# Kernel optimization log

Hardware: AMD Instinct MI355X
Metric: run time of the kernel (lower is better)

The kernel has to match this reference:

```python
import jax, jax.numpy as jnp
import numpy as np

N_HEAD = 16

def setup_inputs() -> dict:
    key = jax.random.key(0)
    k1, k2, k3 = jax.random.split(key, 3)
    B, T, C = 4, 2048, 1024
    x = jax.random.normal(k1, (B, T, C), dtype=jnp.float32)
    W_qkv = jax.random.normal(k2, (3 * C, C), dtype=jnp.float32) * 0.02
    W_o = jax.random.normal(k3, (C, C), dtype=jnp.float32) * (0.02 / np.sqrt(2.0))
    return {"x": x, "W_qkv": W_qkv, "W_o": W_o}

def reference(x, W_qkv, W_o):
    B, T, C = x.shape
    H = N_HEAD
    d_k = C // H
    # combined qkv projection (torch Linear: y = x @ W^T)
    qkv = x @ W_qkv.T                      # (B, T, 3C)
    q, k, v = jnp.split(qkv, 3, axis=-1)
    def split_heads(t):
        return t.reshape(B, T, H, d_k).transpose(0, 2, 1, 3)  # (B, H, T, d_k)
    q, k, v = split_heads(q), split_heads(k), split_heads(v)
    scale = 1.0 / jnp.sqrt(jnp.asarray(d_k, dtype=x.dtype))
    scores = jnp.einsum('bhqd,bhkd->bhqk', q, k) * scale      # (B, H, T, T)
    causal = jnp.tril(jnp.ones((T, T), dtype=bool))           # True = keep
    scores = jnp.where(causal[None, None], scores, -jnp.inf)
    attn = jax.nn.softmax(scores, axis=-1)                    # no NaNs under causal mask
    out = jnp.einsum('bhqk,bhkd->bhqd', attn, v)              # (B, H, T, d_k)
    out = out.transpose(0, 2, 1, 3).reshape(B, T, C)
    return out @ W_o.T
```

## Files before the change

kernel.cpp:

```cpp
#include <hip/hip_runtime.h>
#include <hip/hip_bf16.h>
#include <cstdint>

typedef __bf16 bf16;
typedef __bf16 bf16x8 __attribute__((ext_vector_type(8)));
typedef float f32x4 __attribute__((ext_vector_type(4)));

#define MFMA16(A, B, C) __builtin_amdgcn_mfma_f32_16x16x32_bf16((A), (B), (C), 0, 0, 0)

__device__ __forceinline__ void async16(const bf16* g, bf16* l) {
    __builtin_amdgcn_global_load_lds(
        (const __attribute__((address_space(1))) void*)g,
        (__attribute__((address_space(3))) void*)l, 16, 0, 0);
}

__global__ void cvt_all(const float* __restrict__ x, const float* __restrict__ wq,
                        const float* __restrict__ wo, bf16* __restrict__ xb,
                        bf16* __restrict__ wqb, bf16* __restrict__ wob) {
    const int bid = blockIdx.x;
    const float* s;
    bf16* d;
    int off;
    if (bid < 4096)      { s = x;  d = xb;  off = bid; }
    else if (bid < 5632) { s = wq; d = wqb; off = bid - 4096; }
    else                 { s = wo; d = wob; off = bid - 5632; }
    const size_t i = ((size_t)off * 256 + threadIdx.x) * 8;
    const float4 a = *(const float4*)(s + i);
    const float4 b2 = *(const float4*)(s + i + 4);
    bf16x8 r;
    r[0] = (bf16)a.x; r[1] = (bf16)a.y; r[2] = (bf16)a.z; r[3] = (bf16)a.w;
    r[4] = (bf16)b2.x; r[5] = (bf16)b2.y; r[6] = (bf16)b2.z; r[7] = (bf16)b2.w;
    *(bf16x8*)(d + i) = r;
}

template <int MODE>
__launch_bounds__(256, 3)
__global__ void gemm_nt(const bf16* __restrict__ A, const bf16* __restrict__ Bm,
                        void* __restrict__ O0, bf16* __restrict__ O1,
                        bf16* __restrict__ O2, int N, int K) {
    __shared__ alignas(16) bf16 As[128 * 64];
    __shared__ alignas(16) bf16 Bs[128 * 64];

    const int t = threadIdx.x;
    const int w = t >> 6, l = t & 63, quad = l >> 4, l15 = l & 15;
    const int wm = w & 1, wn = w >> 1;
    const int m0 = blockIdx.y * 128, n0 = blockIdx.x * 128;

    f32x4 acc[4][4] = {};

    const int srow = t >> 3, sch = t & 7;
    const bf16* ga = A + (size_t)(m0 + srow) * K + sch * 8;
    const bf16* gb = Bm + (size_t)(n0 + srow) * K + sch * 8;

    for (int kt = 0; kt < K; kt += 64) {
        __syncthreads();
#pragma unroll
        for (int i = 0; i < 4; i++) {
            async16(ga + (size_t)i * 32 * K + kt, &As[(i * 256 + t) * 8]);
            async16(gb + (size_t)i * 32 * K + kt, &Bs[(i * 256 + t) * 8]);
        }
        __syncthreads();

#pragma unroll
        for (int s = 0; s < 2; s++) {
            bf16x8 af[4], bfr[4];
#pragma unroll
            for (int im = 0; im < 4; im++)
                af[im] = *(const bf16x8*)&As[(wm * 64 + im * 16 + l15) * 64 + s * 32 + quad * 8];
#pragma unroll
            for (int in = 0; in < 4; in++)
                bfr[in] = *(const bf16x8*)&Bs[(wn * 64 + in * 16 + l15) * 64 + s * 32 + quad * 8];
#pragma unroll
            for (int im = 0; im < 4; im++)
#pragma unroll
                for (int in = 0; in < 4; in++)
                    acc[im][in] = MFMA16(af[im], bfr[in], acc[im][in]);
        }
    }

    if (MODE == 0) {
        bf16* Q0 = (bf16*)O0;
#pragma unroll
        for (int in = 0; in < 4; in++) {
            const int n = n0 + wn * 64 + in * 16;
            const int sel = n >> 10;
            const int c = n & 1023;
            const int h = c >> 6;
            const int dd = c & 63;
            bf16* dst = (sel == 0) ? Q0 : ((sel == 1) ? O1 : O2);
#pragma unroll
            for (int im = 0; im < 4; im++) {
#pragma unroll
                for (int r = 0; r < 4; r++) {
                    const int m = m0 + wm * 64 + im * 16 + quad * 4 + r;
                    const int b = m >> 11, tt = m & 2047;
                    dst[((size_t)(b * 16 + h) * 2048 + tt) * 64 + dd + l15] =
                        (bf16)acc[im][in][r];
                }
            }
        }
    } else {
        float* Of = (float*)O0;
#pragma unroll
        for (int im = 0; im < 4; im++) {
#pragma unroll
            for (int in = 0; in < 4; in++) {
#pragma unroll
                for (int r = 0; r < 4; r++) {
                    const int m = m0 + wm * 64 + im * 16 + quad * 4 + r;
                    const int n = n0 + wn * 64 + in * 16 + l15;
                    Of[(size_t)m * N + n] = acc[im][in][r];
                }
            }
        }
    }
}

__launch_bounds__(256, 4)
__global__ void vtrans(const bf16* __restrict__ V, bf16* __restrict__ Vt) {
    __shared__ alignas(16) bf16 Ls[64 * 72];
    const int t = threadIdx.x, bh = blockIdx.y, tt = blockIdx.x;
#pragma unroll
    for (int i = 0; i < 2; i++) {
        const int id = i * 256 + t, r = id >> 3, c = id & 7;
        *(bf16x8*)&Ls[r * 72 + c * 8] =
            *(const bf16x8*)&V[((size_t)bh * 2048 + tt * 64 + r) * 64 + c * 8];
    }
    __syncthreads();
#pragma unroll
    for (int i = 0; i < 2; i++) {
        const int id = i * 256 + t, d = id >> 3, c = id & 7;
        bf16x8 v;
#pragma unroll
        for (int j = 0; j < 8; j++) v[j] = Ls[(c * 8 + j) * 72 + d];
        *(bf16x8*)&Vt[((size_t)bh * 64 + d) * 2048 + tt * 64 + c * 8] = v;
    }
}

__launch_bounds__(256, 4)
__global__ void attn_fwd(const bf16* __restrict__ Q, const bf16* __restrict__ Kk,
                         const bf16* __restrict__ Vt, bf16* __restrict__ O) {
    __shared__ alignas(16) bf16 Ks[64 * 72];
    __shared__ alignas(16) bf16 Vs[64 * 72];

    const int t = threadIdx.x, w = t >> 6, l = t & 63;
    const int quad = l >> 4, l15 = l & 15;
    const int bh = blockIdx.y, pair = blockIdx.x;
    const int b = bh >> 4, h = bh & 15;
    const int sr = t >> 3, sc = t & 7;

    const bf16* Qbase = Q + (size_t)bh * 2048 * 64;
    const bf16* Kbase = Kk + (size_t)bh * 2048 * 64;
    const bf16* Vbase = Vt + (size_t)bh * 64 * 2048;

    const int qt0 = pair, qt1 = 31 - pair;

    int kr[4];
#pragma unroll
    for (int nt = 0; nt < 4; nt++)
        kr[nt] = (nt >> 1) * 32 + (l15 >> 2) * 8 + (nt & 1) * 4 + (l15 & 3);

    bf16x8 aq[2][2];
#pragma unroll
    for (int hf = 0; hf < 2; hf++) {
        const int qrow = (hf ? qt1 : qt0) * 64 + w * 16 + l15;
        aq[hf][0] = *(const bf16x8*)&Qbase[(size_t)qrow * 64 + quad * 8];
        aq[hf][1] = *(const bf16x8*)&Qbase[(size_t)qrow * 64 + 32 + quad * 8];
#pragma unroll
        for (int j = 0; j < 8; j++) {
            aq[hf][0][j] = aq[hf][0][j] * (bf16)0.1803369f;
            aq[hf][1][j] = aq[hf][1][j] * (bf16)0.1803369f;
        }
    }

    bf16x8 ones;
#pragma unroll
    for (int j = 0; j < 8; j++) ones[j] = (bf16)1.0f;

    f32x4 liacc[2] = {};
    f32x4 oa[2][4] = {};

    for (int kt = 0; kt <= qt1; kt++) {
        bf16x8 rk0 = *(const bf16x8*)&Kbase[(size_t)(kt * 64 + sr) * 64 + sc * 8];
        bf16x8 rk1 = *(const bf16x8*)&Kbase[(size_t)(kt * 64 + sr + 32) * 64 + sc * 8];
        bf16x8 rv0 = *(const bf16x8*)&Vbase[(size_t)sr * 2048 + kt * 64 + sc * 8];
        bf16x8 rv1 = *(const bf16x8*)&Vbase[(size_t)(sr + 32) * 2048 + kt * 64 + sc * 8];
        __syncthreads();
        *(bf16x8*)&Ks[sr * 72 + sc * 8] = rk0;
        *(bf16x8*)&Ks[(sr + 32) * 72 + sc * 8] = rk1;
        *(bf16x8*)&Vs[sr * 72 + sc * 8] = rv0;
        *(bf16x8*)&Vs[(sr + 32) * 72 + sc * 8] = rv1;
        __syncthreads();

        const bool do0 = (kt <= qt0);

        bf16x8 ap[2][2];
#pragma unroll
        for (int np = 0; np < 2; np++) {
            bf16x8 ka[2][2];
#pragma unroll
            for (int i = 0; i < 2; i++) {
                ka[i][0] = *(const bf16x8*)&Ks[kr[2 * np + i] * 72 + quad * 8];
                ka[i][1] = *(const bf16x8*)&Ks[kr[2 * np + i] * 72 + 32 + quad * 8];
            }
#pragma unroll
            for (int hf = 0; hf < 2; hf++) {
                if (hf == 0 && !do0) continue;
                const bool diag = (kt == (hf ? qt1 : qt0));
#pragma unroll
                for (int i = 0; i < 2; i++) {
                    f32x4 s = {};
                    s = MFMA16(ka[i][0], aq[hf][0], s);
                    s = MFMA16(ka[i][1], aq[hf][1], s);
                    const int kbase = np * 32 + quad * 8 + i * 4;
#pragma unroll
                    for (int r = 0; r < 4; r++) {
                        float x = s[r];
                        if (diag && (kbase + r) > (w * 16 + l15)) x = -1e30f;
                        ap[hf][np][i * 4 + r] = (bf16)__builtin_amdgcn_exp2f(x);
                    }
                }
            }
        }

#pragma unroll
        for (int s2 = 0; s2 < 2; s2++) {
            if (do0) liacc[0] = MFMA16(ap[0][s2], ones, liacc[0]);
            liacc[1] = MFMA16(ap[1][s2], ones, liacc[1]);
#pragma unroll
            for (int dt = 0; dt < 4; dt++) {
                bf16x8 bv = *(const bf16x8*)&Vs[(dt * 16 + l15) * 72 + s2 * 32 + quad * 8];
                if (do0) oa[0][dt] = MFMA16(ap[0][s2], bv, oa[0][dt]);
                oa[1][dt] = MFMA16(ap[1][s2], bv, oa[1][dt]);
            }
        }
    }

#pragma unroll
    for (int hf = 0; hf < 2; hf++) {
        const int qt = hf ? qt1 : qt0;
#pragma unroll
        for (int r = 0; r < 4; r++) {
            const float inv = __builtin_amdgcn_rcpf(liacc[hf][r]);
            const int m = b * 2048 + qt * 64 + w * 16 + quad * 4 + r;
#pragma unroll
            for (int dt = 0; dt < 4; dt++) {
                O[(size_t)m * 1024 + h * 64 + dt * 16 + l15] = (bf16)(oa[hf][dt][r] * inv);
            }
        }
    }
}

extern "C" void kernel_launch(void* const* d_in, const int* in_sizes, int n_in,
                              void* d_out, int out_size, void* d_ws, size_t ws_size,
                              hipStream_t stream) {
    const float* x = (const float*)d_in[0];
    const float* wqkv = (const float*)d_in[1];
    const float* wo = (const float*)d_in[2];

    const size_t SZ = (size_t)8192 * 1024;
    bf16* xb = (bf16*)d_ws;
    bf16* wqb = xb + SZ;
    bf16* wob = wqb + (size_t)3072 * 1024;
    bf16* Qw = wob + (size_t)1024 * 1024;
    bf16* Kw = Qw + SZ;
    bf16* Vw = Kw + SZ;
    bf16* Vtw = xb;

    dim3 blk(256);
    cvt_all<<<6144, blk, 0, stream>>>(x, wqkv, wo, xb, wqb, wob);
    gemm_nt<0><<<dim3(24, 64), blk, 0, stream>>>(xb, wqb, Qw, Kw, Vw, 3072, 1024);
    vtrans<<<dim3(32, 64), blk, 0, stream>>>(Vw, Vtw);
    attn_fwd<<<dim3(16, 64), blk, 0, stream>>>(Qw, Kw, Vtw, Vw);
    gemm_nt<1><<<dim3(8, 64), blk, 0, stream>>>(Vw, wob, d_out, nullptr, nullptr, 1024, 1024);
}
```

Before: 250.1 us.

## Replace GEMM with double-buffered 128x256 swizzled 512-thread kernel

Rewrites the projection GEMM to use 128x256 tiles with 512 threads and double-buffered LDS. Loads for the next K tile are issued asynchronously, split across two barrier phases so they overlap the MFMAs. LDS chunks are XOR-swizzled to cut bank conflicts, and a block-index remap spreads tiles across XCDs. It also raises wave priority around the MFMA bursts. In exchange it uses more LDS and has fewer blocks per CU, and correctness depends on hand-placed waitcnt counts.

```diff
diff --git a/kernel.cpp b/kernel.cpp
--- a/kernel.cpp
+++ b/kernel.cpp
@@ -34,48 +34,125 @@
 }
 
 template <int MODE>
-__launch_bounds__(256, 3)
-__global__ void gemm_nt(const bf16* __restrict__ A, const bf16* __restrict__ Bm,
+__launch_bounds__(512, 2)
+__global__ void gemm256(const bf16* __restrict__ A, const bf16* __restrict__ Bm,
                         void* __restrict__ O0, bf16* __restrict__ O1,
                         bf16* __restrict__ O2, int N, int K) {
-    __shared__ alignas(16) bf16 As[128 * 64];
-    __shared__ alignas(16) bf16 Bs[128 * 64];
-
-    const int t = threadIdx.x;
-    const int w = t >> 6, l = t & 63, quad = l >> 4, l15 = l & 15;
-    const int wm = w & 1, wn = w >> 1;
-    const int m0 = blockIdx.y * 128, n0 = blockIdx.x * 128;
+    __shared__ alignas(16) bf16 As[2][128 * 64];
+    __shared__ alignas(16) bf16 Bs[2][2][128 * 64];
+
+    const int t = threadIdx.x, w = t >> 6, l = t & 63;
+    const int quad = l >> 4, l15 = l & 15;
+    const int wm = w >> 2, wn = w & 3;
+
+    const int nwg = gridDim.x;
+    const int wg = ((int)blockIdx.x & 7) * (nwg >> 3) + ((int)blockIdx.x >> 3);
+    const int NBN = N >> 8;
+    const int m0 = (wg / NBN) * 128, n0 = (wg % NBN) * 256;
+
+    const int NT = K >> 6;
+
+    int a_src[2], a_dst[2];
+#pragma unroll
+    for (int j = 0; j < 2; j++) {
+        const int id = j * 512 + t;
+        const int row = id >> 3, c = id & 7;
+        a_src[j] = (m0 + row) * K + ((c ^ (row & 7)) << 3);
+        a_dst[j] = id << 3;
+    }
+    int b_src[2], b_h[2], b_dst[2];
+#pragma unroll
+    for (int j = 0; j < 2; j++) {
+        const int id = j * 512 + t;
+        const int u = id >> 8, rr = (id >> 3) & 31, c = id & 7;
+        b_src[j] = (n0 + u * 64 + rr) * K + ((c ^ (rr & 7)) << 3);
+        b_h[j] = u >> 1;
+        b_dst[j] = ((u & 1) << 12) + ((id & 255) << 3);
+    }
+
+    const int sw = l15 & 7;
+    int aoff[4][2], boff[4][2];
+#pragma unroll
+    for (int im = 0; im < 4; im++) {
+        const int r = wm * 64 + im * 16 + l15;
+#pragma unroll
+        for (int s2 = 0; s2 < 2; s2++)
+            aoff[im][s2] = r * 64 + (((s2 * 4 + quad) ^ sw) << 3);
+    }
+    const int bhalf = wn >> 1;
+#pragma unroll
+    for (int in = 0; in < 4; in++) {
+        const int r = (wn & 1) * 64 + (in >> 1) * 32 + (in & 1) * 16 + l15;
+#pragma unroll
+        for (int s2 = 0; s2 < 2; s2++)
+            boff[in][s2] = r * 64 + (((s2 * 4 + quad) ^ sw) << 3);
+    }
 
     f32x4 acc[4][4] = {};
 
-    const int srow = t >> 3, sch = t & 7;
-    const bf16* ga = A + (size_t)(m0 + srow) * K + sch * 8;
-    const bf16* gb = Bm + (size_t)(n0 + srow) * K + sch * 8;
-
-    for (int kt = 0; kt < K; kt += 64) {
-        __syncthreads();
-#pragma unroll
-        for (int i = 0; i < 4; i++) {
-            async16(ga + (size_t)i * 32 * K + kt, &As[(i * 256 + t) * 8]);
-            async16(gb + (size_t)i * 32 * K + kt, &Bs[(i * 256 + t) * 8]);
-        }
-        __syncthreads();
-
-#pragma unroll
-        for (int s = 0; s < 2; s++) {
-            bf16x8 af[4], bfr[4];
-#pragma unroll
-            for (int im = 0; im < 4; im++)
-                af[im] = *(const bf16x8*)&As[(wm * 64 + im * 16 + l15) * 64 + s * 32 + quad * 8];
-#pragma unroll
-            for (int in = 0; in < 4; in++)
-                bfr[in] = *(const bf16x8*)&Bs[(wn * 64 + in * 16 + l15) * 64 + s * 32 + quad * 8];
-#pragma unroll
-            for (int im = 0; im < 4; im++)
-#pragma unroll
-                for (int in = 0; in < 4; in++)
-                    acc[im][in] = MFMA16(af[im], bfr[in], acc[im][in]);
-        }
+    async16(A + a_src[0], &As[0][a_dst[0]]);
+    async16(A + a_src[1], &As[0][a_dst[1]]);
+    async16(Bm + b_src[0], &Bs[0][b_h[0]][b_dst[0]]);
+    async16(Bm + b_src[1], &Bs[0][b_h[1]][b_dst[1]]);
+    async16(Bm + b_src[0] + 32 * K, &Bs[0][b_h[0]][b_dst[0] + 2048]);
+    async16(Bm + b_src[1] + 32 * K, &Bs[0][b_h[1]][b_dst[1] + 2048]);
+
+    for (int tile = 0; tile < NT; ++tile) {
+        const int cb = tile & 1, pb = cb ^ 1;
+        const bool nl = (tile + 1 < NT);
+        const int ks = (tile + 1) << 6;
+
+        asm volatile("s_waitcnt vmcnt(2)" ::: "memory");
+        __builtin_amdgcn_s_barrier();
+        if (nl) {
+            async16(A + a_src[0] + ks, &As[pb][a_dst[0]]);
+            async16(A + a_src[1] + ks, &As[pb][a_dst[1]]);
+            async16(Bm + b_src[0] + ks, &Bs[pb][b_h[0]][b_dst[0]]);
+        }
+        bf16x8 af[4][2], bf0[2][2];
+#pragma unroll
+        for (int im = 0; im < 4; im++)
+#pragma unroll
+            for (int s2 = 0; s2 < 2; s2++)
+                af[im][s2] = *(const bf16x8*)&As[cb][aoff[im][s2]];
+#pragma unroll
+        for (int i2 = 0; i2 < 2; i2++)
+#pragma unroll
+            for (int s2 = 0; s2 < 2; s2++)
+                bf0[i2][s2] = *(const bf16x8*)&Bs[cb][bhalf][boff[i2][s2]];
+        __builtin_amdgcn_s_setprio(1);
+#pragma unroll
+        for (int im = 0; im < 4; im++)
+#pragma unroll
+            for (int i2 = 0; i2 < 2; i2++) {
+                acc[im][i2] = MFMA16(af[im][0], bf0[i2][0], acc[im][i2]);
+                acc[im][i2] = MFMA16(af[im][1], bf0[i2][1], acc[im][i2]);
+            }
+        __builtin_amdgcn_s_setprio(0);
+
+        if (nl) asm volatile("s_waitcnt vmcnt(3)" ::: "memory");
+        else    asm volatile("s_waitcnt vmcnt(0)" ::: "memory");
+        __builtin_amdgcn_s_barrier();
+        if (nl) {
+            async16(Bm + b_src[1] + ks, &Bs[pb][b_h[1]][b_dst[1]]);
+            async16(Bm + b_src[0] + 32 * K + ks, &Bs[pb][b_h[0]][b_dst[0] + 2048]);
+            async16(Bm + b_src[1] + 32 * K + ks, &Bs[pb][b_h[1]][b_dst[1] + 2048]);
+        }
+        bf16x8 bf1[2][2];
+#pragma unroll
+        for (int i2 = 0; i2 < 2; i2++)
+#pragma unroll
+            for (int s2 = 0; s2 < 2; s2++)
+                bf1[i2][s2] = *(const bf16x8*)&Bs[cb][bhalf][boff[2 + i2][s2]];
+        __builtin_amdgcn_s_setprio(1);
+#pragma unroll
+        for (int im = 0; im < 4; im++)
+#pragma unroll
+            for (int i2 = 0; i2 < 2; i2++) {
+                acc[im][2 + i2] = MFMA16(af[im][0], bf1[i2][0], acc[im][2 + i2]);
+                acc[im][2 + i2] = MFMA16(af[im][1], bf1[i2][1], acc[im][2 + i2]);
+            }
+        __builtin_amdgcn_s_setprio(0);
     }
 
     if (MODE == 0) {
@@ -269,8 +346,8 @@
 
     dim3 blk(256);
     cvt_all<<<6144, blk, 0, stream>>>(x, wqkv, wo, xb, wqb, wob);
-    gemm_nt<0><<<dim3(24, 64), blk, 0, stream>>>(xb, wqb, Qw, Kw, Vw, 3072, 1024);
+    gemm256<0><<<dim3(768), dim3(512), 0, stream>>>(xb, wqb, Qw, Kw, Vw, 3072, 1024);
     vtrans<<<dim3(32, 64), blk, 0, stream>>>(Vw, Vtw);
     attn_fwd<<<dim3(16, 64), blk, 0, stream>>>(Qw, Kw, Vtw, Vw);
-    gemm_nt<1><<<dim3(8, 64), blk, 0, stream>>>(Vw, wob, d_out, nullptr, nullptr, 1024, 1024);
-}
+    gemm256<1><<<dim3(256), dim3(512), 0, stream>>>(Vw, wob, d_out, nullptr, nullptr, 1024, 1024);
+}
```

Measured after the change: 274.8 us. 9.9% more time.

## Replace 128x128 GEMM with double-buffered 256x256 tile GEMM using swizzled LDS

Applied to the files above, without the earlier changes.

Rewrites both projection GEMMs to use 256x256 output tiles with 512 threads (8 waves), double-buffered LDS split into k-halves, and global-to-LDS async loads for the next tile interleaved with MFMA on the current one. LDS rows are XOR-swizzled to reduce bank conflicts, and workgroup IDs are remapped across XCDs for L2 locality. The aim is to hide load latency and raise arithmetic intensity in the GEMMs. In exchange it uses 128KB of LDS and more accumulator registers, and the output GEMM launches only 128 workgroups, which may underfill the device.

```diff
diff --git a/kernel.cpp b/kernel.cpp
--- a/kernel.cpp
+++ b/kernel.cpp
@@ -34,86 +34,162 @@
 }
 
 template <int MODE>
-__launch_bounds__(256, 3)
-__global__ void gemm_nt(const bf16* __restrict__ A, const bf16* __restrict__ Bm,
+__launch_bounds__(512, 2)
+__global__ void gemm256(const bf16* __restrict__ A, const bf16* __restrict__ Bm,
                         void* __restrict__ O0, bf16* __restrict__ O1,
                         bf16* __restrict__ O2, int N, int K) {
-    __shared__ alignas(16) bf16 As[128 * 64];
-    __shared__ alignas(16) bf16 Bs[128 * 64];
-
-    const int t = threadIdx.x;
-    const int w = t >> 6, l = t & 63, quad = l >> 4, l15 = l & 15;
-    const int wm = w & 1, wn = w >> 1;
-    const int m0 = blockIdx.y * 128, n0 = blockIdx.x * 128;
-
-    f32x4 acc[4][4] = {};
-
-    const int srow = t >> 3, sch = t & 7;
-    const bf16* ga = A + (size_t)(m0 + srow) * K + sch * 8;
-    const bf16* gb = Bm + (size_t)(n0 + srow) * K + sch * 8;
-
-    for (int kt = 0; kt < K; kt += 64) {
-        __syncthreads();
-#pragma unroll
-        for (int i = 0; i < 4; i++) {
-            async16(ga + (size_t)i * 32 * K + kt, &As[(i * 256 + t) * 8]);
-            async16(gb + (size_t)i * 32 * K + kt, &Bs[(i * 256 + t) * 8]);
-        }
-        __syncthreads();
-
-#pragma unroll
-        for (int s = 0; s < 2; s++) {
-            bf16x8 af[4], bfr[4];
-#pragma unroll
-            for (int im = 0; im < 4; im++)
-                af[im] = *(const bf16x8*)&As[(wm * 64 + im * 16 + l15) * 64 + s * 32 + quad * 8];
-#pragma unroll
-            for (int in = 0; in < 4; in++)
-                bfr[in] = *(const bf16x8*)&Bs[(wn * 64 + in * 16 + l15) * 64 + s * 32 + quad * 8];
-#pragma unroll
-            for (int im = 0; im < 4; im++)
-#pragma unroll
-                for (int in = 0; in < 4; in++)
-                    acc[im][in] = MFMA16(af[im], bfr[in], acc[im][in]);
-        }
+    __shared__ alignas(16) bf16 As[2 * 2 * 8192];
+    __shared__ alignas(16) bf16 Bs[2 * 2 * 8192];
+
+    const int t = threadIdx.x, w = t >> 6, l = t & 63;
+    const int quad = l >> 4, l15 = l & 15;
+    const int wm = w >> 2, wn = w & 3;
+
+    const int nwg = gridDim.x;
+    const int wg = ((int)blockIdx.x & 7) * (nwg >> 3) + ((int)blockIdx.x >> 3);
+    const int NBN = N >> 8;
+    const int m0 = (wg / NBN) * 256, n0 = (wg % NBN) * 256;
+
+    const int NT = K >> 6;
+
+    int a_src[2], b_src[2], sdst[2];
+#pragma unroll
+    for (int jj = 0; jj < 2; jj++) {
+        const int id2 = jj * 512 + t;
+        const int row = id2 >> 2, pc = id2 & 3;
+        const int gcoff = (pc ^ (row & 3)) << 3;
+        a_src[jj] = (m0 + row) * K + gcoff;
+        b_src[jj] = (n0 + row) * K + gcoff;
+        sdst[jj] = id2 << 3;
+    }
+
+    const int pcs = (quad ^ (l15 & 3)) << 3;
+    const int arow = wm * 128 + l15;
+    const int brow = wn * 64 + l15;
+
+    f32x4 acc[8][4] = {};
+
+#define STAGE_A(ktile, buf, kh, jj)                                          \
+    async16(A + a_src[jj] + (ktile) * 64 + (kh) * 32,                        \
+            &As[((((buf) << 1) + (kh)) << 13) + sdst[jj]])
+#define STAGE_B(ktile, buf, kh, jj)                                          \
+    async16(Bm + b_src[jj] + (ktile) * 64 + (kh) * 32,                       \
+            &Bs[((((buf) << 1) + (kh)) << 13) + sdst[jj]])
+
+#define LDA(cb, kh, mf)                                                      \
+    (*(const bf16x8*)&As[((((cb) << 1) + (kh)) << 13) +                      \
+                         ((arow + (mf) * 16) << 5) + pcs])
+#define LDB(cb, kh, nf)                                                      \
+    (*(const bf16x8*)&Bs[((((cb) << 1) + (kh)) << 13) +                      \
+                         ((brow + (nf) * 16) << 5) + pcs])
+
+    STAGE_A(0, 0, 0, 0); STAGE_A(0, 0, 0, 1);
+    STAGE_B(0, 0, 0, 0); STAGE_B(0, 0, 0, 1);
+    STAGE_A(0, 0, 1, 0); STAGE_A(0, 0, 1, 1);
+    STAGE_B(0, 0, 1, 0); STAGE_B(0, 0, 1, 1);
+
+    for (int tile = 0; tile < NT; ++tile) {
+        const int cb = tile & 1, pb = cb ^ 1;
+        const bool nl = (tile + 1 < NT);
+        const int kn = tile + 1;
+        bf16x8 af[4], bfr[4];
+
+        asm volatile("s_waitcnt vmcnt(4)" ::: "memory");
+        __builtin_amdgcn_s_barrier();
+        if (nl) { STAGE_A(kn, pb, 0, 0); STAGE_A(kn, pb, 0, 1); }
+#pragma unroll
+        for (int mf = 0; mf < 4; mf++) af[mf] = LDA(cb, 0, mf);
+#pragma unroll
+        for (int nf = 0; nf < 4; nf++) bfr[nf] = LDB(cb, 0, nf);
+        __builtin_amdgcn_s_setprio(1);
+#pragma unroll
+        for (int mf = 0; mf < 4; mf++)
+#pragma unroll
+            for (int nf = 0; nf < 4; nf++)
+                acc[mf][nf] = MFMA16(af[mf], bfr[nf], acc[mf][nf]);
+        __builtin_amdgcn_s_setprio(0);
+
+        __builtin_amdgcn_s_barrier();
+        if (nl) { STAGE_B(kn, pb, 0, 0); STAGE_B(kn, pb, 0, 1); }
+#pragma unroll
+        for (int mf = 0; mf < 4; mf++) af[mf] = LDA(cb, 0, 4 + mf);
+        __builtin_amdgcn_s_setprio(1);
+#pragma unroll
+        for (int mf = 0; mf < 4; mf++)
+#pragma unroll
+            for (int nf = 0; nf < 4; nf++)
+                acc[4 + mf][nf] = MFMA16(af[mf], bfr[nf], acc[4 + mf][nf]);
+        __builtin_amdgcn_s_setprio(0);
+
+        if (nl) asm volatile("s_waitcnt vmcnt(4)" ::: "memory");
+        else    asm volatile("s_waitcnt vmcnt(0)" ::: "memory");
+        __builtin_amdgcn_s_barrier();
+        if (nl) { STAGE_A(kn, pb, 1, 0); STAGE_A(kn, pb, 1, 1); }
+#pragma unroll
+        for (int mf = 0; mf < 4; mf++) af[mf] = LDA(cb, 1, mf);
+#pragma unroll
+        for (int nf = 0; nf < 4; nf++) bfr[nf] = LDB(cb, 1, nf);
+        __builtin_amdgcn_s_setprio(1);
+#pragma unroll
+        for (int mf = 0; mf < 4; mf++)
+#pragma unroll
+            for (int nf = 0; nf < 4; nf++)
+                acc[mf][nf] = MFMA16(af[mf], bfr[nf], acc[mf][nf]);
+        __builtin_amdgcn_s_setprio(0);
+
+        __builtin_amdgcn_s_barrier();
+        if (nl) { STAGE_B(kn, pb, 1, 0); STAGE_B(kn, pb, 1, 1); }
+#pragma unroll
+        for (int mf = 0; mf < 4; mf++) af[mf] = LDA(cb, 1, 4 + mf);
+        __builtin_amdgcn_s_setprio(1);
+#pragma unroll
+        for (int mf = 0; mf < 4; mf++)
+#pragma unroll
+            for (int nf = 0; nf < 4; nf++)
+                acc[4 + mf][nf] = MFMA16(af[mf], bfr[nf], acc[4 + mf][nf]);
+        __builtin_amdgcn_s_setprio(0);
     }
 
     if (MODE == 0) {
         bf16* Q0 = (bf16*)O0;
 #pragma unroll
-        for (int in = 0; in < 4; in++) {
-            const int n = n0 + wn * 64 + in * 16;
+        for (int nf = 0; nf < 4; nf++) {
+            const int n = n0 + wn * 64 + nf * 16;
             const int sel = n >> 10;
             const int c = n & 1023;
             const int h = c >> 6;
             const int dd = c & 63;
             bf16* dst = (sel == 0) ? Q0 : ((sel == 1) ? O1 : O2);
 #pragma unroll
-            for (int im = 0; im < 4; im++) {
+            for (int mf = 0; mf < 8; mf++) {
 #pragma unroll
                 for (int r = 0; r < 4; r++) {
-                    const int m = m0 + wm * 64 + im * 16 + quad * 4 + r;
+                    const int m = m0 + wm * 128 + mf * 16 + quad * 4 + r;
                     const int b = m >> 11, tt = m & 2047;
                     dst[((size_t)(b * 16 + h) * 2048 + tt) * 64 + dd + l15] =
-                        (bf16)acc[im][in][r];
+                        (bf16)acc[mf][nf][r];
                 }
             }
         }
     } else {
         float* Of = (float*)O0;
 #pragma unroll
-        for (int im = 0; im < 4; im++) {
-#pragma unroll
-            for (int in = 0; in < 4; in++) {
+        for (int mf = 0; mf < 8; mf++) {
+#pragma unroll
+            for (int nf = 0; nf < 4; nf++) {
 #pragma unroll
                 for (int r = 0; r < 4; r++) {
-                    const int m = m0 + wm * 64 + im * 16 + quad * 4 + r;
-                    const int n = n0 + wn * 64 + in * 16 + l15;
-                    Of[(size_t)m * N + n] = acc[im][in][r];
+                    const int m = m0 + wm * 128 + mf * 16 + quad * 4 + r;
+                    const int n = n0 + wn * 64 + nf * 16 + l15;
+                    Of[(size_t)m * N + n] = acc[mf][nf][r];
                 }
             }
         }
     }
+#undef STAGE_A
+#undef STAGE_B
+#undef LDA
+#undef LDB
 }
 
 __launch_bounds__(256, 4)
@@ -269,8 +345,8 @@
 
     dim3 blk(256);
     cvt_all<<<6144, blk, 0, stream>>>(x, wqkv, wo, xb, wqb, wob);
-    gemm_nt<0><<<dim3(24, 64), blk, 0, stream>>>(xb, wqb, Qw, Kw, Vw, 3072, 1024);
+    gemm256<0><<<dim3(384), dim3(512), 0, stream>>>(xb, wqb, Qw, Kw, Vw, 3072, 1024);
     vtrans<<<dim3(32, 64), blk, 0, stream>>>(Vw, Vtw);
     attn_fwd<<<dim3(16, 64), blk, 0, stream>>>(Qw, Kw, Vtw, Vw);
-    gemm_nt<1><<<dim3(8, 64), blk, 0, stream>>>(Vw, wob, d_out, nullptr, nullptr, 1024, 1024);
-}
+    gemm256<1><<<dim3(128), dim3(512), 0, stream>>>(Vw, wob, d_out, nullptr, nullptr, 1024, 1024);
+}
```

New measurement: 280.5 us. 12.2% more time.
